# Kernel tuning notes

Hardware: AMD Instinct MI355X
Metric: run time of the kernel (lower is better)

Reference implementation:

```python
import jax, jax.numpy as jnp
import numpy as np

NUM_NODES = 50000
NUM_EDGES = 800000
NUM_GRAPHS = 64
EMBED = 128
HIDDEN = 128
LAYERS = 3
CLUSTERS = 16
OUT_DIM = 128
MAX_DEG = 64
EPS = 1e-5


def setup_inputs() -> dict:
    key = jax.random.key(0)
    ks = jax.random.split(key, 16)
    deg_idx = jax.random.randint(ks[0], (NUM_NODES,), 0, MAX_DEG + 1)
    edge_index = jax.random.randint(ks[1], (2, NUM_EDGES), 0, NUM_NODES)
    batch = jnp.sort(jax.random.randint(ks[2], (NUM_NODES,), 0, NUM_GRAPHS))
    s = 0.05
    emb = jax.random.normal(ks[3], (MAX_DEG + 1, EMBED), jnp.float32) * s
    Wl = jax.random.normal(ks[4], (LAYERS, HIDDEN, HIDDEN), jnp.float32) * s
    bl = jnp.zeros((LAYERS, HIDDEN), jnp.float32)
    Wr = jax.random.normal(ks[5], (LAYERS, HIDDEN, HIDDEN), jnp.float32) * s
    gamma = jnp.ones((LAYERS, HIDDEN), jnp.float32)
    beta = jnp.zeros((LAYERS, HIDDEN), jnp.float32)
    attn_W = jax.random.normal(ks[6], (HIDDEN, CLUSTERS), jnp.float32) * s
    attn_b = jnp.zeros((CLUSTERS,), jnp.float32)
    out_W = jax.random.normal(ks[7], (HIDDEN, OUT_DIM), jnp.float32) * s
    out_b = jnp.zeros((OUT_DIM,), jnp.float32)
    return {"emb": emb, "Wl": Wl, "bl": bl, "Wr": Wr, "gamma": gamma,
            "beta": beta, "attn_W": attn_W, "attn_b": attn_b,
            "out_W": out_W, "out_b": out_b, "deg_idx": deg_idx,
            "edge_index": edge_index, "batch": batch}


def reference(emb, Wl, bl, Wr, gamma, beta, attn_W, attn_b, out_W, out_b,
              deg_idx, edge_index, batch):
    N = deg_idx.shape[0]
    src, dst = edge_index[0], edge_index[1]
    x = emb[deg_idx]  # [N, EMBED]
    for l in range(Wl.shape[0]):
        # SAGEConv (mean aggr): lin_l(mean_j x_j) + lin_r(x); lin_r has no bias
        msg_sum = jax.ops.segment_sum(x[src], dst, num_segments=N)
        cnt = jax.ops.segment_sum(jnp.ones((src.shape[0], 1), x.dtype), dst,
                                  num_segments=N)
        mean = msg_sum / jnp.maximum(cnt, 1.0)
        x = mean @ Wl[l] + bl[l] + x @ Wr[l]
        # BatchNorm1d (training-mode batch stats, biased variance)
        mu = x.mean(axis=0)
        var = jnp.mean((x - mu) ** 2, axis=0)
        x = (x - mu) * jax.lax.rsqrt(var + EPS) * gamma[l] + beta[l]
        x = jax.nn.relu(x)  # dropout is identity in eval
    scores = x @ attn_W + attn_b  # [N, C] (num_heads == 1 -> squeeze)
    # per-graph softmax over nodes (segment softmax along dim 0)
    smax = jax.ops.segment_max(scores, batch, num_segments=NUM_GRAPHS)
    e = jnp.exp(scores - smax[batch])
    denom = jax.ops.segment_sum(e, batch, num_segments=NUM_GRAPHS)
    w = e / denom[batch]  # [N, C]
    # c_b = w_b^T @ x_b  -> segment-weighted sums: [B, C, H]
    clust = jax.ops.segment_sum(w[:, :, None] * x[:, None, :], batch,
                                num_segments=NUM_GRAPHS)
    return clust @ out_W + out_b  # [B, C, OUT_DIM]
```

## Files before the change

### kernel.cpp

```cpp
#include <hip/hip_runtime.h>

typedef unsigned short u16;
typedef unsigned int   u32;

#define H    128
#define C    16
#define ODIM 128

typedef short bf16x8 __attribute__((ext_vector_type(8)));
typedef float f32x4  __attribute__((ext_vector_type(4)));
typedef float f32x2v __attribute__((ext_vector_type(2)));

#define WSP 272
#define NP  256

__device__ __forceinline__ float bf2f(u32 v){
  union { u32 i; float f; } t; t.i = v << 16; return t.f;
}
__device__ __forceinline__ u16 f2bf(float f){
  u32 u = __float_as_uint(f);
  u32 r = u + 0x7fffu + ((u >> 16) & 1u);
  return (u16)(r >> 16);
}
__device__ __forceinline__ u32 pack2(float a, float b){
  return (u32)f2bf(a) | ((u32)f2bf(b) << 16);
}
__device__ __forceinline__ u32 pack_fp8x4(float a, float b, float c, float d){
  int p = __builtin_amdgcn_cvt_pk_fp8_f32(a, b, 0, false);
  p     = __builtin_amdgcn_cvt_pk_fp8_f32(c, d, p, true);
  return (u32)p;
}

__global__ __launch_bounds__(256) void k_setup(const float* __restrict__ emb,
    const int* __restrict__ deg, u16* __restrict__ xb, u32* __restrict__ xq,
    const int* __restrict__ batch, int* __restrict__ gs,
    const float* __restrict__ Wl, const float* __restrict__ Wr,
    u16* __restrict__ Wt, const int* __restrict__ ei,
    int* __restrict__ blkhist, int N, int B, int NB, int E, int chunk,
    int g0, int g1, int g2){
  __shared__ __align__(16) char smem[4608];
  int bid = blockIdx.x, tid = threadIdx.x;
  if (bid < g0){
    int i = bid*256 + tid;
    if (i < N*32){
      int n = i >> 5, q = i & 31;
      int d = deg[n];
      float4 v = ((const float4*)(emb + (size_t)d*H))[q];
      uint2 o; o.x = pack2(v.x, v.y); o.y = pack2(v.z, v.w);
      ((uint2*)(xb + (size_t)n*H))[q] = o;
      xq[i] = pack_fp8x4(v.x, v.y, v.z, v.w);
    }
  } else if (bid < g1){
    int n = (bid - g0)*256 + tid;
    if (n < N){
      int b = batch[n];
      if (n == 0){ for (int g = 0; g <= b; g++) gs[g] = 0; }
      else {
        int pb = batch[n-1];
        for (int g = pb+1; g <= b; g++) gs[g] = n;
      }
      if (n == N-1){ for (int g = b+1; g <= B; g++) gs[g] = N; }
    }
  } else if (bid < g2){
    u16 (*T)[18] = (u16(*)[18])smem;
    int b = bid - g1;
    int strip = b & 7, half = (b >> 3) & 1, l = b >> 4;
    const float* M = (half ? Wr : Wl) + (size_t)l*H*H;
    int k0 = strip * 16;
    #pragma unroll
    for (int j = 0; j < 8; j++){
      int u = tid + j*256;
      int kk = u >> 7, h = u & 127;
      T[h][kk] = f2bf(M[(size_t)(k0 + kk)*H + h]);
    }
    __syncthreads();
    #pragma unroll
    for (int j = 0; j < 8; j++){
      int u = tid + j*256;
      int h = u >> 4, k16 = u & 15;
      Wt[((size_t)(l*H + h))*256 + half*128 + k0 + k16] = T[h][k16];
    }
  } else {
    int* hist = (int*)smem;
    int blk = bid - g2;
    for (int b = tid; b < NB; b += 256) hist[b] = 0;
    __syncthreads();
    int start = blk*chunk, end = min(E, start + chunk);
    for (int e = start + tid; e < end; e += 256)
      atomicAdd(&hist[ei[E + e] >> 7], 1);
    __syncthreads();
    for (int b = tid; b < NB; b += 256) blkhist[b*NP + blk] = hist[b];
  }
}

__global__ __launch_bounds__(256) void k_scanA(const int* __restrict__ in,
    int* __restrict__ out, int* __restrict__ bsum, int n){
  __shared__ int wsum[4];
  int tid = threadIdx.x;
  int base = blockIdx.x*1024 + tid*4;
  int v0 = (base+0 < n) ? in[base+0] : 0;
  int v1 = (base+1 < n) ? in[base+1] : 0;
  int v2 = (base+2 < n) ? in[base+2] : 0;
  int v3 = (base+3 < n) ? in[base+3] : 0;
  int tsum = v0+v1+v2+v3;
  int lane = tid & 63, w = tid >> 6;
  int incl = tsum;
  for (int d = 1; d < 64; d <<= 1){
    int t = __shfl_up(incl, d, 64);
    if (lane >= d) incl += t;
  }
  if (lane == 63) wsum[w] = incl;
  __syncthreads();
  int woff = 0;
  for (int i = 0; i < w; i++) woff += wsum[i];
  int excl = woff + incl - tsum;
  if (base+0 < n) out[base+0] = excl;
  if (base+1 < n) out[base+1] = excl + v0;
  if (base+2 < n) out[base+2] = excl + v0 + v1;
  if (base+3 < n) out[base+3] = excl + v0 + v1 + v2;
  if (tid == 255) bsum[blockIdx.x] = woff + incl;
}

__global__ __launch_bounds__(256) void k_scanB(const int* __restrict__ bsum,
    int* __restrict__ boff, int nb){
  __shared__ int ws[4];
  int tid = threadIdx.x;
  int v = (tid < nb) ? bsum[tid] : 0;
  int lane = tid & 63, w = tid >> 6;
  int incl = v;
  for (int d = 1; d < 64; d <<= 1){
    int t = __shfl_up(incl, d, 64);
    if (lane >= d) incl += t;
  }
  if (lane == 63) ws[w] = incl;
  __syncthreads();
  int woff = 0;
  for (int i = 0; i < w; i++) woff += ws[i];
  boff[tid] = woff + incl - v;
}

__global__ __launch_bounds__(256) void k_place(const int* __restrict__ ei,
    const int* __restrict__ bases, const int* __restrict__ boff,
    int2* __restrict__ pairs, int NB, int E, int chunk){
  __shared__ int cursor[400];
  int blk = blockIdx.x, tid = threadIdx.x;
  for (int b = tid; b < NB; b += 256){
    int i = b*NP + blk;
    cursor[b] = bases[i] + boff[i >> 10];
  }
  __syncthreads();
  int start = blk*chunk, end = min(E, start + chunk);
  for (int e = start + tid; e < end; e += 256){
    int s = ei[e], d = ei[E + e];
    int pos = atomicAdd(&cursor[d >> 7], 1);
    pairs[pos] = make_int2(s, d);
  }
}

__global__ __launch_bounds__(256) void k_cnt_place(const int2* __restrict__ pairs,
    const int* __restrict__ bases, const int* __restrict__ boff,
    int* __restrict__ rowptr, int* __restrict__ col, int NB, int N, int E){
  int b = blockIdx.x, tid = threadIdx.x;
  int i0 = b*NP;
  int bstart = bases[i0] + boff[i0 >> 10];
  int bend = E;
  if (b+1 < NB){ int i1 = (b+1)*NP; bend = bases[i1] + boff[i1 >> 10]; }
  __shared__ int cnt[128], sc[128], rank[128];
  if (tid < 128) cnt[tid] = 0;
  __syncthreads();
  for (int e = bstart + tid; e < bend; e += 256)
    atomicAdd(&cnt[pairs[e].y & 127], 1);
  __syncthreads();
  if (tid < 128) sc[tid] = cnt[tid];
  for (int d = 1; d < 128; d <<= 1){
    int v = 0;
    __syncthreads();
    if (tid < 128 && tid >= d) v = sc[tid - d];
    __syncthreads();
    if (tid < 128) sc[tid] += v;
  }
  __syncthreads();
  if (tid < 128){
    int excl = sc[tid] - cnt[tid];
    rank[tid] = bstart + excl;
    int node = b*128 + tid;
    if (node < N) rowptr[node] = bstart + excl;
  }
  if (b == NB-1 && tid == 0) rowptr[N] = E;
  __syncthreads();
  for (int e = bstart + tid; e < bend; e += 256){
    int2 p = pairs[e];
    int pos = atomicAdd(&rank[p.y & 127], 1);
    col[pos] = p.x;
  }
}

__device__ __forceinline__ void dec16(float* a, uint4 v){
  f32x2v p;
  p = __builtin_amdgcn_cvt_pk_f32_fp8((int)v.x, false); a[0]+=p.x; a[1]+=p.y;
  p = __builtin_amdgcn_cvt_pk_f32_fp8((int)v.x, true ); a[2]+=p.x; a[3]+=p.y;
  p = __builtin_amdgcn_cvt_pk_f32_fp8((int)v.y, false); a[4]+=p.x; a[5]+=p.y;
  p = __builtin_amdgcn_cvt_pk_f32_fp8((int)v.y, true ); a[6]+=p.x; a[7]+=p.y;
  p = __builtin_amdgcn_cvt_pk_f32_fp8((int)v.z, false); a[8]+=p.x; a[9]+=p.y;
  p = __builtin_amdgcn_cvt_pk_f32_fp8((int)v.z, true ); a[10]+=p.x; a[11]+=p.y;
  p = __builtin_amdgcn_cvt_pk_f32_fp8((int)v.w, false); a[12]+=p.x; a[13]+=p.y;
  p = __builtin_amdgcn_cvt_pk_f32_fp8((int)v.w, true ); a[14]+=p.x; a[15]+=p.y;
}

__global__ __launch_bounds__(256) void k_agg(const u32* __restrict__ xq,
    const int* __restrict__ rowptr, const int* __restrict__ col,
    u16* __restrict__ meanb, int N){
  int wid  = (blockIdx.x*256 + threadIdx.x) >> 6;
  int lane = threadIdx.x & 63;
  if (wid >= N) return;
  int r0 = rowptr[wid], r1 = rowptr[wid+1];
  int grp = lane >> 3, fl = lane & 7;
  const u32* xf = xq + fl*4;
  float a[16];
  #pragma unroll
  for (int j = 0; j < 16; j++) a[j] = 0.f;
  int e = r0 + grp;
  for (; e + 8 < r1; e += 16){
    uint4 v = *(const uint4*)(xf + (size_t)col[e]*32);
    uint4 u = *(const uint4*)(xf + (size_t)col[e+8]*32);
    dec16(a, v);
    dec16(a, u);
  }
  if (e < r1){
    uint4 v = *(const uint4*)(xf + (size_t)col[e]*32);
    dec16(a, v);
  }
  #pragma unroll
  for (int j = 0; j < 16; j++){
    a[j] += __shfl_xor(a[j], 8, 64);
    a[j] += __shfl_xor(a[j], 16, 64);
    a[j] += __shfl_xor(a[j], 32, 64);
  }
  if (grp == 0){
    float invc = 1.0f / (float)max(r1 - r0, 1);
    uint4 o0, o1;
    o0.x = pack2(a[0]*invc,  a[1]*invc);
    o0.y = pack2(a[2]*invc,  a[3]*invc);
    o0.z = pack2(a[4]*invc,  a[5]*invc);
    o0.w = pack2(a[6]*invc,  a[7]*invc);
    o1.x = pack2(a[8]*invc,  a[9]*invc);
    o1.y = pack2(a[10]*invc, a[11]*invc);
    o1.z = pack2(a[12]*invc, a[13]*invc);
    o1.w = pack2(a[14]*invc, a[15]*invc);
    u16* mp = meanb + (size_t)wid*H + fl*16;
    *(uint4*)mp       = o0;
    *(uint4*)(mp + 8) = o1;
  }
}

__global__ __launch_bounds__(256) void k_linear(const u16* __restrict__ meanb,
    const u16* __restrict__ xb, const u16* __restrict__ Wt,
    const float* __restrict__ bl, float* __restrict__ x2,
    float* __restrict__ pstats, int N){
  __shared__ u16 Ws[128][WSP];
  __shared__ float Sh[128], Qh[128];
  int tid = threadIdx.x;
  if (tid < 128){ Sh[tid] = 0.f; Qh[tid] = 0.f; }
  int lane = tid & 63, w = tid >> 6;
  int mlane = lane & 15, quad = lane >> 4;
  int node = blockIdx.x*64 + w*16 + mlane;
  const u16* arow_m = meanb + (size_t)node*H + quad*8;
  const u16* arow_x = xb   + (size_t)node*H + quad*8;
  bf16x8 af[8];
  #pragma unroll
  for (int kk = 0; kk < 4; kk++){
    af[kk]     = *(const bf16x8*)(arow_m + kk*32);
    af[kk + 4] = *(const bf16x8*)(arow_x + kk*32);
  }
  #pragma unroll
  for (int j = 0; j < 16; j++){
    int u = tid + j*256;
    int row = u >> 5, seg = u & 31;
    uint4 v = ((const uint4*)(Wt + (size_t)row*256))[seg];
    *(uint4*)&Ws[row][seg*8] = v;
  }
  __syncthreads();
  f32x4 acc[8];
  #pragma unroll
  for (int t = 0; t < 8; t++) acc[t] = (f32x4){0.f, 0.f, 0.f, 0.f};
  #pragma unroll
  for (int kk = 0; kk < 8; kk++){
    #pragma unroll
    for (int t = 0; t < 8; t++){
      bf16x8 b = *(const bf16x8*)&Ws[t*16 + mlane][kk*32 + quad*8];
      acc[t] = __builtin_amdgcn_mfma_f32_16x16x32_bf16(af[kk], b, acc[t], 0, 0, 0);
    }
  }
  #pragma unroll
  for (int t = 0; t < 8; t++){
    int h = t*16 + mlane;
    float bv = bl[h];
    float s = 0.f, q = 0.f;
    #pragma unroll
    for (int r = 0; r < 4; r++){
      int nd = blockIdx.x*64 + w*16 + quad*4 + r;
      if (nd < N){
        float v = acc[t][r] + bv;
        x2[(size_t)nd*H + h] = v;
        s += v; q = fmaf(v, v, q);
      }
    }
    s += __shfl_xor(s, 16, 64); s += __shfl_xor(s, 32, 64);
    q += __shfl_xor(q, 16, 64); q += __shfl_xor(q, 32, 64);
    if (quad == 0){
      atomicAdd(&Sh[h], s);
      atomicAdd(&Qh[h], q);
    }
  }
  __syncthreads();
  {
    float v = (tid < 128) ? Sh[tid] : Qh[tid - 128];
    pstats[(size_t)blockIdx.x*256 + tid] = v;
  }
}

__global__ __launch_bounds__(256) void k_statred(const float* __restrict__ pstats,
    float* __restrict__ stats, int nblk){
  __shared__ float red[4];
  int c = blockIdx.x, tid = threadIdx.x;
  float s = 0.f;
  for (int b = tid; b < nblk; b += 256)
    s += pstats[(size_t)b*256 + c];
  s += __shfl_xor(s, 1, 64);  s += __shfl_xor(s, 2, 64);
  s += __shfl_xor(s, 4, 64);  s += __shfl_xor(s, 8, 64);
  s += __shfl_xor(s, 16, 64); s += __shfl_xor(s, 32, 64);
  if ((tid & 63) == 0) red[tid >> 6] = s;
  __syncthreads();
  if (tid == 0) stats[c] = red[0] + red[1] + red[2] + red[3];
}

__global__ __launch_bounds__(256) void k_bnrelu(const float* __restrict__ x2,
    const float* __restrict__ stats, const float* __restrict__ gamma,
    const float* __restrict__ beta, u16* __restrict__ xb, u32* __restrict__ xq,
    int N, float invN,
    const float* __restrict__ attn_W, const float* __restrict__ attn_b,
    float* __restrict__ escore, int do_scores){
  __shared__ float xs[8][132];
  __shared__ float aw[H*C];
  __shared__ float ab[C];
  int tid = threadIdx.x;
  int i = blockIdx.x*256 + tid;
  bool active = (i < N*32);
  int h = (tid & 31) * 4;
  float r[4] = {0.f, 0.f, 0.f, 0.f};
  if (active){
    float4 v = ((const float4*)x2)[i];
    float vv[4] = {v.x, v.y, v.z, v.w};
    #pragma unroll
    for (int j = 0; j < 4; j++){
      float mu  = stats[h+j] * invN;
      float var = fmaf(-mu, mu, stats[H + h + j] * invN);
      float sc  = rsqrtf(var + 1e-5f) * gamma[h+j];
      float bi  = beta[h+j];
      r[j] = fmaxf(fmaf(vv[j] - mu, sc, bi), 0.0f);
    }
    uint2 o; o.x = pack2(r[0], r[1]); o.y = pack2(r[2], r[3]);
    ((uint2*)xb)[i] = o;
    xq[i] = pack_fp8x4(r[0], r[1], r[2], r[3]);
  }
  if (do_scores){
    #pragma unroll
    for (int j = 0; j < 8; j++) aw[tid + j*256] = attn_W[tid + j*256];
    if (tid < C) ab[tid] = attn_b[tid];
    int ln = tid >> 5;
    if (active){
      xs[ln][h+0]=r[0]; xs[ln][h+1]=r[1]; xs[ln][h+2]=r[2]; xs[ln][h+3]=r[3];
    }
    __syncthreads();
    if (tid < 128){
      int n2 = tid >> 4, c = tid & 15;
      int node = blockIdx.x*8 + n2;
      if (node < N){
        float acc = ab[c];
        #pragma unroll 4
        for (int k = 0; k < H; k++)
          acc = fmaf(xs[n2][k], aw[k*C + c], acc);
        escore[(size_t)node*C + c] = __expf(acc);
      }
    }
  }
}

__global__ __launch_bounds__(256) void k_clust(const u16* __restrict__ xb,
    const float* __restrict__ escore, const int* __restrict__ gs,
    float* __restrict__ partial){
  int g = blockIdx.x >> 4, b = blockIdx.x & 15;
  int h = threadIdx.x & 127, cg = threadIdx.x >> 7;
  int a = gs[g], e2 = gs[g+1];
  float acc[8] = {0,0,0,0,0,0,0,0};
  for (int n = a + b; n < e2; n += 16){
    float xv = bf2f(xb[(size_t)n*H + h]);
    const float4* ep = (const float4*)(escore + (size_t)n*C) + cg*2;
    float4 e0 = ep[0], e1 = ep[1];
    acc[0] = fmaf(e0.x, xv, acc[0]);
    acc[1] = fmaf(e0.y, xv, acc[1]);
    acc[2] = fmaf(e0.z, xv, acc[2]);
    acc[3] = fmaf(e0.w, xv, acc[3]);
    acc[4] = fmaf(e1.x, xv, acc[4]);
    acc[5] = fmaf(e1.y, xv, acc[5]);
    acc[6] = fmaf(e1.z, xv, acc[6]);
    acc[7] = fmaf(e1.w, xv, acc[7]);
  }
  int c0 = cg*8;
  float* dst = partial + (((size_t)(g*16 + b))*C)*H + h;
  #pragma unroll
  for (int r = 0; r < 8; r++)
    dst[(size_t)(c0 + r)*H] = acc[r];
}

__global__ __launch_bounds__(256) void k_out(const float* __restrict__ partial,
    const float* __restrict__ escore, const int* __restrict__ gs,
    const float* __restrict__ out_W, const float* __restrict__ out_b,
    float* __restrict__ out){
  __shared__ float cs[2][128];
  __shared__ float dsum[4];
  int tid = threadIdx.x;
  int r = tid >> 7, h = tid & 127;
  int row = blockIdx.x*2 + r;
  int g = row >> 4, c = row & 15;
  int a = gs[g], b2 = gs[g+1];
  float s = 0.f;
  for (int n = a + h; n < b2; n += 128) s += escore[(size_t)n*C + c];
  s += __shfl_xor(s, 1, 64);  s += __shfl_xor(s, 2, 64);
  s += __shfl_xor(s, 4, 64);  s += __shfl_xor(s, 8, 64);
  s += __shfl_xor(s, 16, 64); s += __shfl_xor(s, 32, 64);
  if ((tid & 63) == 0) dsum[tid >> 6] = s;
  float p = 0.f;
  for (int b = 0; b < 16; b++)
    p += partial[(((size_t)(g*16 + b))*C + c)*H + h];
  cs[r][h] = p;
  __syncthreads();
  float gden = dsum[r*2] + dsum[r*2 + 1];
  float inv = gden > 0.f ? 1.0f / gden : 0.f;
  float acc = 0.f;
  for (int hh = 0; hh < H; hh++)
    acc = fmaf(cs[r][hh], out_W[hh*ODIM + h], acc);
  out[(size_t)row*ODIM + h] = fmaf(acc, inv, out_b[h]);
}

extern "C" void kernel_launch(void* const* d_in, const int* in_sizes, int n_in,
                              void* d_out, int out_size, void* d_ws, size_t ws_size,
                              hipStream_t stream){
  const float* emb    = (const float*)d_in[0];
  const float* Wl     = (const float*)d_in[1];
  const float* bl     = (const float*)d_in[2];
  const float* Wr     = (const float*)d_in[3];
  const float* gamma  = (const float*)d_in[4];
  const float* beta   = (const float*)d_in[5];
  const float* attn_W = (const float*)d_in[6];
  const float* attn_b = (const float*)d_in[7];
  const float* out_W  = (const float*)d_in[8];
  const float* out_b  = (const float*)d_in[9];
  const int* deg    = (const int*)d_in[10];
  const int* ei     = (const int*)d_in[11];
  const int* batch  = (const int*)d_in[12];
  float* out = (float*)d_out;

  const int N = in_sizes[10];
  const int E = in_sizes[11] / 2;
  const int L = in_sizes[1] / (H*H);
  const int B = out_size / (C*ODIM);
  const int NB = (N + 127) >> 7;
  const int nbh = NB * NP;
  const int chunk = (E + NP - 1) / NP;
  const int nblkL = (N + 63) / 64;

  size_t off = 0;
  auto alloc = [&](size_t bytes) -> void* {
    void* p = (char*)d_ws + off;
    off += (bytes + 255) & ~(size_t)255;
    return p;
  };
  u16*   xb     = (u16*)  alloc((size_t)N*H*2);
  u32*   xq     = (u32*)  alloc((size_t)N*H);
  u16*   meanb  = (u16*)  alloc((size_t)N*H*2);
  float* x2     = (float*)alloc((size_t)N*H*4);
  int2*  pairs  = (int2*)x2;
  float* partial= x2;
  u16*   Wt     = (u16*)  alloc((size_t)L*H*256*2);
  float* escore = (float*)alloc((size_t)N*C*4);
  int*   col    = (int*)  alloc((size_t)E*4);
  int*   rowptr = (int*)  alloc((size_t)(N+1)*4);
  int*   blkhist= (int*)  alloc((size_t)nbh*4);
  int*   bases  = (int*)  alloc((size_t)nbh*4);
  int*   bsum   = (int*)  alloc(256*4);
  int*   boff   = (int*)  alloc(256*4);
  int*   gs     = (int*)  alloc((size_t)(B+1)*4);
  float* stats  = (float*)alloc((size_t)L*2*H*4);
  float* pstats = (float*)alloc((size_t)nblkL*256*4);

  int g0 = (N*32 + 255)/256;
  int g1 = g0 + (N + 255)/256;
  int g2 = g1 + L*16;
  int gT = g2 + NP;
  hipLaunchKernelGGL(k_setup, dim3(gT), dim3(256), 0, stream,
                     emb, deg, xb, xq, batch, gs, Wl, Wr, Wt, ei, blkhist,
                     N, B, NB, E, chunk, g0, g1, g2);
  int nblkS = (nbh + 1023) / 1024;
  hipLaunchKernelGGL(k_scanA,  dim3(nblkS), dim3(256), 0, stream, blkhist, bases, bsum, nbh);
  hipLaunchKernelGGL(k_scanB,  dim3(1),     dim3(256), 0, stream, bsum, boff, nblkS);
  hipLaunchKernelGGL(k_place,  dim3(NP), dim3(256), 0, stream, ei, bases, boff, pairs, NB, E, chunk);
  hipLaunchKernelGGL(k_cnt_place, dim3(NB), dim3(256), 0, stream, pairs, bases, boff, rowptr, col, NB, N, E);

  float invN = 1.0f / (float)N;
  for (int l = 0; l < L; l++){
    hipLaunchKernelGGL(k_agg,    dim3((N+3)/4),  dim3(256), 0, stream, xq, rowptr, col, meanb, N);
    hipLaunchKernelGGL(k_linear, dim3(nblkL),    dim3(256), 0, stream,
                       meanb, xb, Wt + (size_t)l*H*256, bl + (size_t)l*H, x2,
                       pstats, N);
    hipLaunchKernelGGL(k_statred,dim3(256),      dim3(256), 0, stream, pstats, stats + l*2*H, nblkL);
    hipLaunchKernelGGL(k_bnrelu, dim3((N*32+255)/256), dim3(256), 0, stream,
                       x2, stats + l*2*H, gamma + (size_t)l*H, beta + (size_t)l*H,
                       xb, xq, N, invN, attn_W, attn_b, escore, (l == L-1) ? 1 : 0);
  }
  hipLaunchKernelGGL(k_clust,  dim3(B*16),  dim3(256), 0, stream, xb, escore, gs, partial);
  hipLaunchKernelGGL(k_out,    dim3(B*C/2), dim3(256), 0, stream, partial, escore, gs, out_W, out_b, out);
}
```

Measured before the change: 334.0 us.

## Fold reduction kernels into producers via last-block counters and store pre-BN activations as bf16

Removes the k_scanB, k_statred and k_out launches. The last block to finish k_scanA, k_linear and k_clust, detected through an atomic counter, now does that kernel's tail work. The pre-BatchNorm activations x2 are stored as bf16 instead of fp32, halving that intermediate's write and read traffic. The aggregation accumulators are rewritten as float2 vectors, which may enable packed adds. The cost is serial tail work inside a single block (for example, one block sums all pstats rows), plus a bf16 rounding of the pre-BN values and reliance on threadfence/atomic ordering.

Result: slower. 1.047 ms (+213.4%).

```diff
diff --git a/kernel.cpp b/kernel.cpp
--- a/kernel.cpp
+++ b/kernel.cpp
@@ -30,14 +30,16 @@
   p     = __builtin_amdgcn_cvt_pk_fp8_f32(c, d, p, true);
   return (u32)p;
 }
+
+#define NCTR 68
 
 __global__ __launch_bounds__(256) void k_setup(const float* __restrict__ emb,
     const int* __restrict__ deg, u16* __restrict__ xb, u32* __restrict__ xq,
     const int* __restrict__ batch, int* __restrict__ gs,
     const float* __restrict__ Wl, const float* __restrict__ Wr,
     u16* __restrict__ Wt, const int* __restrict__ ei,
-    int* __restrict__ blkhist, int N, int B, int NB, int E, int chunk,
-    int g0, int g1, int g2){
+    int* __restrict__ blkhist, int* __restrict__ counters,
+    int N, int B, int NB, int E, int chunk, int g0, int g1, int g2){
   __shared__ __align__(16) char smem[4608];
   int bid = blockIdx.x, tid = threadIdx.x;
   if (bid < g0){
@@ -51,6 +53,7 @@
       xq[i] = pack_fp8x4(v.x, v.y, v.z, v.w);
     }
   } else if (bid < g1){
+    if (bid == g0 && tid < NCTR) counters[tid] = 0;
     int n = (bid - g0)*256 + tid;
     if (n < N){
       int b = batch[n];
@@ -94,8 +97,10 @@
 }
 
 __global__ __launch_bounds__(256) void k_scanA(const int* __restrict__ in,
-    int* __restrict__ out, int* __restrict__ bsum, int n){
+    int* __restrict__ out, int* __restrict__ bsum, int* __restrict__ boff,
+    int* __restrict__ counters, int n){
   __shared__ int wsum[4];
+  __shared__ int lastflag;
   int tid = threadIdx.x;
   int base = blockIdx.x*1024 + tid*4;
   int v0 = (base+0 < n) ? in[base+0] : 0;
@@ -119,24 +124,27 @@
   if (base+2 < n) out[base+2] = excl + v0 + v1;
   if (base+3 < n) out[base+3] = excl + v0 + v1 + v2;
   if (tid == 255) bsum[blockIdx.x] = woff + incl;
-}
-
-__global__ __launch_bounds__(256) void k_scanB(const int* __restrict__ bsum,
-    int* __restrict__ boff, int nb){
-  __shared__ int ws[4];
-  int tid = threadIdx.x;
-  int v = (tid < nb) ? bsum[tid] : 0;
-  int lane = tid & 63, w = tid >> 6;
-  int incl = v;
-  for (int d = 1; d < 64; d <<= 1){
-    int t = __shfl_up(incl, d, 64);
-    if (lane >= d) incl += t;
-  }
-  if (lane == 63) ws[w] = incl;
-  __syncthreads();
-  int woff = 0;
-  for (int i = 0; i < w; i++) woff += ws[i];
-  boff[tid] = woff + incl - v;
+  __syncthreads();
+  if (tid == 0){
+    __threadfence();
+    lastflag = (atomicAdd(&counters[0], 1) == (int)gridDim.x - 1);
+  }
+  __syncthreads();
+  if (lastflag){
+    __threadfence();
+    int nb = gridDim.x;
+    int v = (tid < nb) ? bsum[tid] : 0;
+    int incl2 = v;
+    for (int d = 1; d < 64; d <<= 1){
+      int t = __shfl_up(incl2, d, 64);
+      if (lane >= d) incl2 += t;
+    }
+    if (lane == 63) wsum[w] = incl2;
+    __syncthreads();
+    int woff2 = 0;
+    for (int i = 0; i < w; i++) woff2 += wsum[i];
+    if (tid < nb) boff[tid] = woff2 + incl2 - v;
+  }
 }
 
 __global__ __launch_bounds__(256) void k_place(const int* __restrict__ ei,
@@ -195,16 +203,15 @@
   }
 }
 
-__device__ __forceinline__ void dec16(float* a, uint4 v){
-  f32x2v p;
-  p = __builtin_amdgcn_cvt_pk_f32_fp8((int)v.x, false); a[0]+=p.x; a[1]+=p.y;
-  p = __builtin_amdgcn_cvt_pk_f32_fp8((int)v.x, true ); a[2]+=p.x; a[3]+=p.y;
-  p = __builtin_amdgcn_cvt_pk_f32_fp8((int)v.y, false); a[4]+=p.x; a[5]+=p.y;
-  p = __builtin_amdgcn_cvt_pk_f32_fp8((int)v.y, true ); a[6]+=p.x; a[7]+=p.y;
-  p = __builtin_amdgcn_cvt_pk_f32_fp8((int)v.z, false); a[8]+=p.x; a[9]+=p.y;
-  p = __builtin_amdgcn_cvt_pk_f32_fp8((int)v.z, true ); a[10]+=p.x; a[11]+=p.y;
-  p = __builtin_amdgcn_cvt_pk_f32_fp8((int)v.w, false); a[12]+=p.x; a[13]+=p.y;
-  p = __builtin_amdgcn_cvt_pk_f32_fp8((int)v.w, true ); a[14]+=p.x; a[15]+=p.y;
+__device__ __forceinline__ void dec16v(f32x2v* a, uint4 v){
+  a[0] += __builtin_amdgcn_cvt_pk_f32_fp8((int)v.x, false);
+  a[1] += __builtin_amdgcn_cvt_pk_f32_fp8((int)v.x, true );
+  a[2] += __builtin_amdgcn_cvt_pk_f32_fp8((int)v.y, false);
+  a[3] += __builtin_amdgcn_cvt_pk_f32_fp8((int)v.y, true );
+  a[4] += __builtin_amdgcn_cvt_pk_f32_fp8((int)v.z, false);
+  a[5] += __builtin_amdgcn_cvt_pk_f32_fp8((int)v.z, true );
+  a[6] += __builtin_amdgcn_cvt_pk_f32_fp8((int)v.w, false);
+  a[7] += __builtin_amdgcn_cvt_pk_f32_fp8((int)v.w, true );
 }
 
 __global__ __launch_bounds__(256) void k_agg(const u32* __restrict__ xq,
@@ -216,37 +223,37 @@
   int r0 = rowptr[wid], r1 = rowptr[wid+1];
   int grp = lane >> 3, fl = lane & 7;
   const u32* xf = xq + fl*4;
-  float a[16];
-  #pragma unroll
-  for (int j = 0; j < 16; j++) a[j] = 0.f;
+  f32x2v a[8];
+  #pragma unroll
+  for (int j = 0; j < 8; j++) a[j] = (f32x2v){0.f, 0.f};
   int e = r0 + grp;
   for (; e + 8 < r1; e += 16){
     uint4 v = *(const uint4*)(xf + (size_t)col[e]*32);
     uint4 u = *(const uint4*)(xf + (size_t)col[e+8]*32);
-    dec16(a, v);
-    dec16(a, u);
+    dec16v(a, v);
+    dec16v(a, u);
   }
   if (e < r1){
     uint4 v = *(const uint4*)(xf + (size_t)col[e]*32);
-    dec16(a, v);
-  }
-  #pragma unroll
-  for (int j = 0; j < 16; j++){
-    a[j] += __shfl_xor(a[j], 8, 64);
-    a[j] += __shfl_xor(a[j], 16, 64);
-    a[j] += __shfl_xor(a[j], 32, 64);
+    dec16v(a, v);
+  }
+  #pragma unroll
+  for (int j = 0; j < 8; j++){
+    a[j].x += __shfl_xor(a[j].x, 8, 64);  a[j].y += __shfl_xor(a[j].y, 8, 64);
+    a[j].x += __shfl_xor(a[j].x, 16, 64); a[j].y += __shfl_xor(a[j].y, 16, 64);
+    a[j].x += __shfl_xor(a[j].x, 32, 64); a[j].y += __shfl_xor(a[j].y, 32, 64);
   }
   if (grp == 0){
     float invc = 1.0f / (float)max(r1 - r0, 1);
     uint4 o0, o1;
-    o0.x = pack2(a[0]*invc,  a[1]*invc);
-    o0.y = pack2(a[2]*invc,  a[3]*invc);
-    o0.z = pack2(a[4]*invc,  a[5]*invc);
-    o0.w = pack2(a[6]*invc,  a[7]*invc);
-    o1.x = pack2(a[8]*invc,  a[9]*invc);
-    o1.y = pack2(a[10]*invc, a[11]*invc);
-    o1.z = pack2(a[12]*invc, a[13]*invc);
-    o1.w = pack2(a[14]*invc, a[15]*invc);
+    o0.x = pack2(a[0].x*invc, a[0].y*invc);
+    o0.y = pack2(a[1].x*invc, a[1].y*invc);
+    o0.z = pack2(a[2].x*invc, a[2].y*invc);
+    o0.w = pack2(a[3].x*invc, a[3].y*invc);
+    o1.x = pack2(a[4].x*invc, a[4].y*invc);
+    o1.y = pack2(a[5].x*invc, a[5].y*invc);
+    o1.z = pack2(a[6].x*invc, a[6].y*invc);
+    o1.w = pack2(a[7].x*invc, a[7].y*invc);
     u16* mp = meanb + (size_t)wid*H + fl*16;
     *(uint4*)mp       = o0;
     *(uint4*)(mp + 8) = o1;
@@ -255,10 +262,12 @@
 
 __global__ __launch_bounds__(256) void k_linear(const u16* __restrict__ meanb,
     const u16* __restrict__ xb, const u16* __restrict__ Wt,
-    const float* __restrict__ bl, float* __restrict__ x2,
-    float* __restrict__ pstats, int N){
+    const float* __restrict__ bl, u16* __restrict__ x2b,
+    float* __restrict__ pstats, float* __restrict__ stats,
+    int* __restrict__ counters, int l, int N){
   __shared__ u16 Ws[128][WSP];
   __shared__ float Sh[128], Qh[128];
+  __shared__ int lastflag;
   int tid = threadIdx.x;
   if (tid < 128){ Sh[tid] = 0.f; Qh[tid] = 0.f; }
   int lane = tid & 63, w = tid >> 6;
@@ -301,7 +310,7 @@
       int nd = blockIdx.x*64 + w*16 + quad*4 + r;
       if (nd < N){
         float v = acc[t][r] + bv;
-        x2[(size_t)nd*H + h] = v;
+        x2b[(size_t)nd*H + h] = f2bf(v);
         s += v; q = fmaf(v, v, q);
       }
     }
@@ -317,24 +326,23 @@
     float v = (tid < 128) ? Sh[tid] : Qh[tid - 128];
     pstats[(size_t)blockIdx.x*256 + tid] = v;
   }
-}
-
-__global__ __launch_bounds__(256) void k_statred(const float* __restrict__ pstats,
-    float* __restrict__ stats, int nblk){
-  __shared__ float red[4];
-  int c = blockIdx.x, tid = threadIdx.x;
-  float s = 0.f;
-  for (int b = tid; b < nblk; b += 256)
-    s += pstats[(size_t)b*256 + c];
-  s += __shfl_xor(s, 1, 64);  s += __shfl_xor(s, 2, 64);
-  s += __shfl_xor(s, 4, 64);  s += __shfl_xor(s, 8, 64);
-  s += __shfl_xor(s, 16, 64); s += __shfl_xor(s, 32, 64);
-  if ((tid & 63) == 0) red[tid >> 6] = s;
-  __syncthreads();
-  if (tid == 0) stats[c] = red[0] + red[1] + red[2] + red[3];
-}
-
-__global__ __launch_bounds__(256) void k_bnrelu(const float* __restrict__ x2,
+  __syncthreads();
+  if (tid == 0){
+    __threadfence();
+    lastflag = (atomicAdd(&counters[1 + l], 1) == (int)gridDim.x - 1);
+  }
+  __syncthreads();
+  if (lastflag){
+    __threadfence();
+    int nblk = gridDim.x;
+    float s = 0.f;
+    for (int b = 0; b < nblk; b++)
+      s += pstats[(size_t)b*256 + tid];
+    stats[tid] = s;
+  }
+}
+
+__global__ __launch_bounds__(256) void k_bnrelu(const u16* __restrict__ x2b,
     const float* __restrict__ stats, const float* __restrict__ gamma,
     const float* __restrict__ beta, u16* __restrict__ xb, u32* __restrict__ xq,
     int N, float invN,
@@ -349,8 +357,9 @@
   int h = (tid & 31) * 4;
   float r[4] = {0.f, 0.f, 0.f, 0.f};
   if (active){
-    float4 v = ((const float4*)x2)[i];
-    float vv[4] = {v.x, v.y, v.z, v.w};
+    uint2 o2 = ((const uint2*)x2b)[i];
+    float vv[4] = {bf2f(o2.x & 0xffff), bf2f(o2.x >> 16),
+                   bf2f(o2.y & 0xffff), bf2f(o2.y >> 16)};
     #pragma unroll
     for (int j = 0; j < 4; j++){
       float mu  = stats[h+j] * invN;
@@ -388,9 +397,16 @@
 
 __global__ __launch_bounds__(256) void k_clust(const u16* __restrict__ xb,
     const float* __restrict__ escore, const int* __restrict__ gs,
-    float* __restrict__ partial){
+    float* __restrict__ partial, int* __restrict__ counters,
+    const float* __restrict__ out_W, const float* __restrict__ out_b,
+    float* __restrict__ out){
+  __shared__ float cs[16][129];
+  __shared__ float dpart[16][17];
+  __shared__ float dinv[16];
+  __shared__ int lastflag;
   int g = blockIdx.x >> 4, b = blockIdx.x & 15;
-  int h = threadIdx.x & 127, cg = threadIdx.x >> 7;
+  int tid = threadIdx.x;
+  int h = tid & 127, cg = tid >> 7;
   int a = gs[g], e2 = gs[g+1];
   float acc[8] = {0,0,0,0,0,0,0,0};
   for (int n = a + b; n < e2; n += 16){
@@ -411,36 +427,44 @@
   #pragma unroll
   for (int r = 0; r < 8; r++)
     dst[(size_t)(c0 + r)*H] = acc[r];
-}
-
-__global__ __launch_bounds__(256) void k_out(const float* __restrict__ partial,
-    const float* __restrict__ escore, const int* __restrict__ gs,
-    const float* __restrict__ out_W, const float* __restrict__ out_b,
-    float* __restrict__ out){
-  __shared__ float cs[2][128];
-  __shared__ float dsum[4];
-  int tid = threadIdx.x;
-  int r = tid >> 7, h = tid & 127;
-  int row = blockIdx.x*2 + r;
-  int g = row >> 4, c = row & 15;
-  int a = gs[g], b2 = gs[g+1];
-  float s = 0.f;
-  for (int n = a + h; n < b2; n += 128) s += escore[(size_t)n*C + c];
-  s += __shfl_xor(s, 1, 64);  s += __shfl_xor(s, 2, 64);
-  s += __shfl_xor(s, 4, 64);  s += __shfl_xor(s, 8, 64);
-  s += __shfl_xor(s, 16, 64); s += __shfl_xor(s, 32, 64);
-  if ((tid & 63) == 0) dsum[tid >> 6] = s;
-  float p = 0.f;
-  for (int b = 0; b < 16; b++)
-    p += partial[(((size_t)(g*16 + b))*C + c)*H + h];
-  cs[r][h] = p;
-  __syncthreads();
-  float gden = dsum[r*2] + dsum[r*2 + 1];
-  float inv = gden > 0.f ? 1.0f / gden : 0.f;
-  float acc = 0.f;
-  for (int hh = 0; hh < H; hh++)
-    acc = fmaf(cs[r][hh], out_W[hh*ODIM + h], acc);
-  out[(size_t)row*ODIM + h] = fmaf(acc, inv, out_b[h]);
+  __syncthreads();
+  if (tid == 0){
+    __threadfence();
+    lastflag = (atomicAdd(&counters[4 + g], 1) == 15);
+  }
+  __syncthreads();
+  if (!lastflag) return;
+  __threadfence();
+  for (int u = tid; u < C*H; u += 256){
+    int c = u >> 7, hh = u & 127;
+    float s = 0.f;
+    #pragma unroll 4
+    for (int b2 = 0; b2 < 16; b2++)
+      s += partial[(((size_t)(g*16 + b2))*C + c)*H + hh];
+    cs[c][hh] = s;
+  }
+  {
+    int c = tid & 15, sub = tid >> 4;
+    float s = 0.f;
+    for (int n = a + sub; n < e2; n += 16) s += escore[(size_t)n*C + c];
+    dpart[sub][c] = s;
+    __syncthreads();
+    if (tid < 16){
+      float t2 = 0.f;
+      #pragma unroll
+      for (int sb = 0; sb < 16; sb++) t2 += dpart[sb][tid];
+      dinv[tid] = t2 > 0.f ? 1.0f/t2 : 0.f;
+    }
+  }
+  __syncthreads();
+  for (int u = tid; u < C*ODIM; u += 256){
+    int c = u >> 7, o = u & 127;
+    float acc2 = 0.f;
+    #pragma unroll 4
+    for (int hh = 0; hh < H; hh++)
+      acc2 = fmaf(cs[c][hh], out_W[hh*ODIM + o], acc2);
+    out[((size_t)(g*16 + c))*ODIM + o] = fmaf(acc2, dinv[c], out_b[o]);
+  }
 }
 
 extern "C" void kernel_launch(void* const* d_in, const int* in_sizes, int n_in,
@@ -479,9 +503,9 @@
   u16*   xb     = (u16*)  alloc((size_t)N*H*2);
   u32*   xq     = (u32*)  alloc((size_t)N*H);
   u16*   meanb  = (u16*)  alloc((size_t)N*H*2);
-  float* x2     = (float*)alloc((size_t)N*H*4);
-  int2*  pairs  = (int2*)x2;
-  float* partial= x2;
+  u16*   x2b    = (u16*)  alloc((size_t)N*H*2);
+  int2*  pairs  = (int2*)x2b;
+  float* partial= (float*)x2b;
   u16*   Wt     = (u16*)  alloc((size_t)L*H*256*2);
   float* escore = (float*)alloc((size_t)N*C*4);
   int*   col    = (int*)  alloc((size_t)E*4);
@@ -493,6 +517,7 @@
   int*   gs     = (int*)  alloc((size_t)(B+1)*4);
   float* stats  = (float*)alloc((size_t)L*2*H*4);
   float* pstats = (float*)alloc((size_t)nblkL*256*4);
+  int*   counters=(int*)  alloc(NCTR*4);
 
   int g0 = (N*32 + 255)/256;
   int g1 = g0 + (N + 255)/256;
@@ -500,24 +525,25 @@
   int gT = g2 + NP;
   hipLaunchKernelGGL(k_setup, dim3(gT), dim3(256), 0, stream,
                      emb, deg, xb, xq, batch, gs, Wl, Wr, Wt, ei, blkhist,
-                     N, B, NB, E, chunk, g0, g1, g2);
+                     counters, N, B, NB, E, chunk, g0, g1, g2);
   int nblkS = (nbh + 1023) / 1024;
-  hipLaunchKernelGGL(k_scanA,  dim3(nblkS), dim3(256), 0, stream, blkhist, bases, bsum, nbh);
-  hipLaunchKernelGGL(k_scanB,  dim3(1),     dim3(256), 0, stream, bsum, boff, nblkS);
-  hipLaunchKernelGGL(k_place,  dim3(NP), dim3(256), 0, stream, ei, bases, boff, pairs, NB, E, chunk);
-  hipLaunchKernelGGL(k_cnt_place, dim3(NB), dim3(256), 0, stream, pairs, bases, boff, rowptr, col, NB, N, E);
+  hipLaunchKernelGGL(k_scanA, dim3(nblkS), dim3(256), 0, stream,
+                     blkhist, bases, bsum, boff, counters, nbh);
+  hipLaunchKernelGGL(k_place, dim3(NP), dim3(256), 0, stream,
+                     ei, bases, boff, pairs, NB, E, chunk);
+  hipLaunchKernelGGL(k_cnt_place, dim3(NB), dim3(256), 0, stream,
+                     pairs, bases, boff, rowptr, col, NB, N, E);
 
   float invN = 1.0f / (float)N;
   for (int l = 0; l < L; l++){
     hipLaunchKernelGGL(k_agg,    dim3((N+3)/4),  dim3(256), 0, stream, xq, rowptr, col, meanb, N);
     hipLaunchKernelGGL(k_linear, dim3(nblkL),    dim3(256), 0, stream,
-                       meanb, xb, Wt + (size_t)l*H*256, bl + (size_t)l*H, x2,
-                       pstats, N);
-    hipLaunchKernelGGL(k_statred,dim3(256),      dim3(256), 0, stream, pstats, stats + l*2*H, nblkL);
+                       meanb, xb, Wt + (size_t)l*H*256, bl + (size_t)l*H, x2b,
+                       pstats, stats + l*2*H, counters, l, N);
     hipLaunchKernelGGL(k_bnrelu, dim3((N*32+255)/256), dim3(256), 0, stream,
-                       x2, stats + l*2*H, gamma + (size_t)l*H, beta + (size_t)l*H,
+                       x2b, stats + l*2*H, gamma + (size_t)l*H, beta + (size_t)l*H,
                        xb, xq, N, invN, attn_W, attn_b, escore, (l == L-1) ? 1 : 0);
   }
-  hipLaunchKernelGGL(k_clust,  dim3(B*16),  dim3(256), 0, stream, xb, escore, gs, partial);
-  hipLaunchKernelGGL(k_out,    dim3(B*C/2), dim3(256), 0, stream, partial, escore, gs, out_W, out_b, out);
-}
+  hipLaunchKernelGGL(k_clust, dim3(B*16), dim3(256), 0, stream,
+                     xb, escore, gs, partial, counters, out_W, out_b, out);
+}
```
